# Kernel tuning notes

Measured on AMD Instinct MI355X. Metric: run time of the kernel, lower is better.

## Reference

```python
import jax, jax.numpy as jnp
import numpy as np

N0 = 292864   # input (hop-2) nodes
N1 = 11264    # hop-1 nodes
B = 1024      # target nodes
F_IN, HID, OUT = 128, 256, 47
E0, E1 = 281600, 10240
H_HIT = 146432
N_CACHE, N_GLOBAL, C_FEAT = 50000, 100000, 200000
P = 2048


def setup_inputs() -> dict:
    key = jax.random.key(0)
    ks = jax.random.split(key, 20)
    perm = jax.random.permutation(ks[0], N0)
    hit_pos = perm[:H_HIT]
    miss_pos = perm[H_HIT:]
    x = jax.random.normal(ks[1], (N0 - H_HIT, F_IN), jnp.float32)
    feat_cache = jax.random.normal(ks[2], (C_FEAT, F_IN), jnp.float32)
    hit_idx = jax.random.randint(ks[3], (H_HIT,), 0, C_FEAT)
    edge_index0 = jnp.stack([jax.random.randint(ks[4], (E0,), 0, N0),
                             jax.random.randint(ks[5], (E0,), 0, N1)])
    edge_index1 = jnp.stack([jax.random.randint(ks[6], (E1,), 0, N1),
                             jax.random.randint(ks[7], (E1,), 0, B)])
    emb_cache = jax.random.normal(ks[8], (N_CACHE, HID), jnp.float32)
    emb_cache_table = jax.random.randint(ks[9], (N_GLOBAL,), 0, N_CACHE)
    push_batch_id = jax.random.randint(ks[10], (P,), 0, N1)
    push_global_id = jax.random.randint(ks[11], (P,), 0, N_GLOBAL)
    pull_batch_id = jax.random.randint(ks[12], (P,), 0, N1)
    pull_global_id = jax.random.randint(ks[13], (P,), 0, N_GLOBAL)
    W0_l = jax.random.normal(ks[14], (F_IN, HID), jnp.float32) / np.sqrt(F_IN)
    b0_l = jnp.zeros((HID,), jnp.float32)
    W0_r = jax.random.normal(ks[15], (F_IN, HID), jnp.float32) / np.sqrt(F_IN)
    W1_l = jax.random.normal(ks[16], (HID, OUT), jnp.float32) / np.sqrt(HID)
    b1_l = jnp.zeros((OUT,), jnp.float32)
    W1_r = jax.random.normal(ks[17], (HID, OUT), jnp.float32) / np.sqrt(HID)
    return dict(x=x, feat_cache=feat_cache, emb_cache=emb_cache, hit_idx=hit_idx,
                hit_pos=hit_pos, miss_pos=miss_pos, edge_index0=edge_index0,
                edge_index1=edge_index1, emb_cache_table=emb_cache_table,
                push_batch_id=push_batch_id, push_global_id=push_global_id,
                pull_batch_id=pull_batch_id, pull_global_id=pull_global_id,
                W0_l=W0_l, b0_l=b0_l, W0_r=W0_r, W1_l=W1_l, b1_l=b1_l, W1_r=W1_r)


def _sage_conv(h_src, h_dst, edge_index, n_dst, W_l, b_l, W_r):
    # PyG SAGEConv (mean aggr): out = lin_l(mean_j x_j) + lin_r(x_i)
    src, dst = edge_index[0], edge_index[1]
    msg = h_src[src]                                              # [E, F] gather
    s = jax.ops.segment_sum(msg, dst, num_segments=n_dst)        # scatter-add
    cnt = jax.ops.segment_sum(jnp.ones((src.shape[0],), h_src.dtype), dst,
                              num_segments=n_dst)[:, None]
    mean = s / jnp.maximum(cnt, 1.0)
    return mean @ W_l + b_l + h_dst @ W_r


def reference(x, feat_cache, emb_cache, hit_idx, hit_pos, miss_pos,
              edge_index0, edge_index1, emb_cache_table,
              push_batch_id, push_global_id, pull_batch_id, pull_global_id,
              W0_l, b0_l, W0_r, W1_l, b1_l, W1_r):
    # Assemble node features from pinned feature cache (hits) + fetched feats (misses)
    h = jnp.zeros((N0, F_IN), x.dtype)
    h = h.at[hit_pos].set(feat_cache[hit_idx]).at[miss_pos].set(x)
    # Layer 0 (inner hop)
    h = _sage_conv(h, h[:N1], edge_index0, N1, W0_l, b0_l, W0_r)
    h = jax.nn.relu(h)  # dropout p=0.5 skipped (eval mode)
    # Last layer: push stale embeddings into cache, then pull cached embeddings
    slots_push = emb_cache_table[push_global_id]
    emb_cache = emb_cache.at[slots_push].set(jax.lax.stop_gradient(h[push_batch_id]))
    pulled = jax.lax.stop_gradient(emb_cache[emb_cache_table[pull_global_id]])
    h = h.at[pull_batch_id].set(pulled)
    out = _sage_conv(h, h[:B], edge_index1, B, W1_l, b1_l, W1_r)
    return jax.nn.log_softmax(out, axis=-1)
```

## Files before the change

### kernel.cpp

```cpp
#include <hip/hip_runtime.h>
#include <math.h>

#define N0c     292864
#define N1c     11264
#define Bc      1024
#define F_INc   128
#define HIDc    256
#define OUTc    47
#define E0c     281600
#define E1c     10240
#define H_HITc  146432
#define N_CACHEc 50000
#define C_FEATc 200000
#define Pc      2048

__global__ void prep_kernel(const int* __restrict__ hit_pos, const int* __restrict__ hit_idx,
                            const int* __restrict__ miss_pos, int* __restrict__ map,
                            int* __restrict__ cur0, int* __restrict__ pwin,
                            int* __restrict__ cur1, int* __restrict__ win,
                            int* __restrict__ src_row) {
  int i = blockIdx.x * 256 + threadIdx.x;
  if (i < H_HITc) {
    map[hit_pos[i]]  = hit_idx[i];
    map[miss_pos[i]] = C_FEATc + i;
  }
  if (i < N1c) { cur0[i] = 0; pwin[i] = -1; src_row[i] = i; }
  if (i < Bc)  cur1[i] = 0;
  if (i < N_CACHEc) win[i] = -1;
}

__global__ void atomics_kernel(const int* __restrict__ e0, const int* __restrict__ e1,
                               int* __restrict__ deg0, int* __restrict__ deg1,
                               const int* __restrict__ push_gid, const int* __restrict__ table,
                               int* __restrict__ win,
                               const int* __restrict__ pull_bid, int* __restrict__ pwin) {
  int i = blockIdx.x * 256 + threadIdx.x;
  if (i < E0c) {
    atomicAdd(&deg0[e0[E0c + i]], 1);
  } else if (i < E0c + E1c) {
    int j = i - E0c;
    atomicAdd(&deg1[e1[E1c + j]], 1);
  } else if (i < E0c + E1c + Pc) {
    int j = i - E0c - E1c;
    atomicMax(&win[table[push_gid[j]]], j);
  } else if (i < E0c + E1c + 2 * Pc) {
    int j = i - E0c - E1c - Pc;
    atomicMax(&pwin[pull_bid[j]], j);
  }
}

__device__ void scan_block(const int* __restrict__ deg, int* __restrict__ off,
                           int* __restrict__ cur, int n) {
  __shared__ int wsum[16];
  int tid = threadIdx.x;
  int lane = tid & 63, wid = tid >> 6;
  int ITEMS = (n + 1023) >> 10;
  int base = tid * ITEMS;
  int v[12];
  int sum = 0;
  for (int j = 0; j < ITEMS; ++j) {
    int i = base + j;
    v[j] = (i < n) ? deg[i] : 0;
    sum += v[j];
  }
  int s = sum;
  for (int o = 1; o < 64; o <<= 1) {
    int t = __shfl_up(s, o);
    if (lane >= o) s += t;
  }
  if (lane == 63) wsum[wid] = s;
  __syncthreads();
  if (tid < 16) {
    int w = wsum[tid];
    for (int o = 1; o < 16; o <<= 1) {
      int t = __shfl_up(w, o);
      if (tid >= o) w += t;
    }
    wsum[tid] = w;
  }
  __syncthreads();
  int wbase = (wid > 0) ? wsum[wid - 1] : 0;
  int run = wbase + s - sum;
  for (int j = 0; j < ITEMS; ++j) {
    int i = base + j;
    if (i < n) { off[i] = run; cur[i] = run; run += v[j]; }
  }
  if (tid == 1023) off[n] = run;
}

__global__ __launch_bounds__(1024) void scan_both_kernel(
    int* __restrict__ cur0, int* __restrict__ off0,
    int* __restrict__ cur1, int* __restrict__ off1) {
  if (blockIdx.x == 0) scan_block(cur0, off0, cur0, N1c);
  else                 scan_block(cur1, off1, cur1, Bc);
}

__global__ void scatter_resolve_kernel(const int* __restrict__ e0, const int* __restrict__ e1,
                                       const int* __restrict__ map,
                                       int* __restrict__ cur0, int* __restrict__ esrc0,
                                       int* __restrict__ cur1, int* __restrict__ esrc1,
                                       const int* __restrict__ pull_bid, const int* __restrict__ pull_gid,
                                       const int* __restrict__ table, const int* __restrict__ win,
                                       const int* __restrict__ pwin, const int* __restrict__ push_bid,
                                       int* __restrict__ src_row) {
  int i = blockIdx.x * 256 + threadIdx.x;
  if (i < E0c) {
    int p = atomicAdd(&cur0[e0[E0c + i]], 1);
    esrc0[p] = map[e0[i]];
  } else if (i < E0c + E1c) {
    int j = i - E0c;
    int p = atomicAdd(&cur1[e1[E1c + j]], 1);
    esrc1[p] = e1[j];
  } else if (i < E0c + E1c + Pc) {
    int j = i - E0c - E1c;
    int b = pull_bid[j];
    if (pwin[b] == j) {
      int slot = table[pull_gid[j]];
      int w = win[slot];
      src_row[b] = (w >= 0) ? push_bid[w] : (N1c + slot);
    }
  }
}

__global__ __launch_bounds__(256) void agg1_kernel(
    const int* __restrict__ off, const int* __restrict__ esrc,
    const float* __restrict__ fc, const float* __restrict__ x,
    float4* __restrict__ mean4) {
  __shared__ float4 sbuf[8][32];
  int d = blockIdx.x;
  int slot = threadIdx.x >> 5, lane = threadIdx.x & 31;
  int s = off[d], e = off[d + 1];
  float4 a0 = make_float4(0.f, 0.f, 0.f, 0.f);
  float4 a1 = a0, a2 = a0, a3 = a0;
  int i0 = s + slot, i1 = i0 + 8, i2 = i0 + 16, i3 = i0 + 24;
  int m0 = (i0 < e) ? esrc[i0] : -1;
  int m1 = (i1 < e) ? esrc[i1] : -1;
  int m2 = (i2 < e) ? esrc[i2] : -1;
  int m3 = (i3 < e) ? esrc[i3] : -1;
  while (i0 < e) {
    int n0 = i0 + 32, n1 = i1 + 32, n2 = i2 + 32, n3 = i3 + 32;
    int p0 = (n0 < e) ? esrc[n0] : -1;
    int p1 = (n1 < e) ? esrc[n1] : -1;
    int p2 = (n2 < e) ? esrc[n2] : -1;
    int p3 = (n3 < e) ? esrc[n3] : -1;
    {
      const float* r = (m0 < C_FEATc) ? (fc + (size_t)m0 * F_INc)
                                      : (x + (size_t)(m0 - C_FEATc) * F_INc);
      float4 v = ((const float4*)r)[lane];
      a0.x += v.x; a0.y += v.y; a0.z += v.z; a0.w += v.w;
    }
    if (i1 < e) {
      const float* r = (m1 < C_FEATc) ? (fc + (size_t)m1 * F_INc)
                                      : (x + (size_t)(m1 - C_FEATc) * F_INc);
      float4 v = ((const float4*)r)[lane];
      a1.x += v.x; a1.y += v.y; a1.z += v.z; a1.w += v.w;
    }
    if (i2 < e) {
      const float* r = (m2 < C_FEATc) ? (fc + (size_t)m2 * F_INc)
                                      : (x + (size_t)(m2 - C_FEATc) * F_INc);
      float4 v = ((const float4*)r)[lane];
      a2.x += v.x; a2.y += v.y; a2.z += v.z; a2.w += v.w;
    }
    if (i3 < e) {
      const float* r = (m3 < C_FEATc) ? (fc + (size_t)m3 * F_INc)
                                      : (x + (size_t)(m3 - C_FEATc) * F_INc);
      float4 v = ((const float4*)r)[lane];
      a3.x += v.x; a3.y += v.y; a3.z += v.z; a3.w += v.w;
    }
    i0 = n0; m0 = p0; i1 = n1; m1 = p1; i2 = n2; m2 = p2; i3 = n3; m3 = p3;
  }
  a0.x += a1.x + a2.x + a3.x;
  a0.y += a1.y + a2.y + a3.y;
  a0.z += a1.z + a2.z + a3.z;
  a0.w += a1.w + a2.w + a3.w;
  sbuf[slot][lane] = a0;
  __syncthreads();
  if (slot < 4) {
    float4 o = sbuf[slot + 4][lane];
    a0.x += o.x; a0.y += o.y; a0.z += o.z; a0.w += o.w;
    sbuf[slot][lane] = a0;
  }
  __syncthreads();
  if (slot < 2) {
    float4 o = sbuf[slot + 2][lane];
    a0.x += o.x; a0.y += o.y; a0.z += o.z; a0.w += o.w;
    sbuf[slot][lane] = a0;
  }
  __syncthreads();
  if (slot == 0) {
    float4 o = sbuf[1][lane];
    a0.x += o.x; a0.y += o.y; a0.z += o.z; a0.w += o.w;
    float inv = 1.f / fmaxf((float)(e - s), 1.f);
    mean4[(size_t)d * 32 + lane] = make_float4(a0.x * inv, a0.y * inv,
                                               a0.z * inv, a0.w * inv);
  }
}

#define ROWS1 16
__global__ __launch_bounds__(256) void gemm1_kernel(
    const float4* __restrict__ mean4, const int* __restrict__ map,
    const float* __restrict__ fc, const float* __restrict__ x,
    const float* __restrict__ W0l, const float* __restrict__ b0,
    const float* __restrict__ W0r, float* __restrict__ h1) {
  __shared__ float lin[ROWS1][256];
  int g0 = blockIdx.x * ROWS1;
  int tid = threadIdx.x;
  for (int idx = tid; idx < ROWS1 * 32; idx += 256) {
    int r = idx >> 5, l = idx & 31;
    ((float4*)&lin[r][0])[l] = mean4[(size_t)(g0 + r) * 32 + l];
  }
  for (int idx = tid; idx < ROWS1 * 32; idx += 256) {
    int r = idx >> 5, l = idx & 31;
    int m = map[g0 + r];
    const float* row = (m < C_FEATc) ? (fc + (size_t)m * F_INc)
                                     : (x + (size_t)(m - C_FEATc) * F_INc);
    ((float4*)&lin[r][128])[l] = ((const float4*)row)[l];
  }
  __syncthreads();
  int col = tid;
  float acc[ROWS1];
#pragma unroll
  for (int r = 0; r < ROWS1; ++r) acc[r] = 0.f;
  for (int kb = 0; kb < 32; ++kb) {
    float w0 = W0l[(kb * 4 + 0) * 256 + col];
    float w1 = W0l[(kb * 4 + 1) * 256 + col];
    float w2 = W0l[(kb * 4 + 2) * 256 + col];
    float w3 = W0l[(kb * 4 + 3) * 256 + col];
#pragma unroll
    for (int r = 0; r < ROWS1; ++r) {
      float4 a = *(const float4*)&lin[r][kb * 4];
      acc[r] += a.x * w0 + a.y * w1 + a.z * w2 + a.w * w3;
    }
  }
  for (int kb = 0; kb < 32; ++kb) {
    float w0 = W0r[(kb * 4 + 0) * 256 + col];
    float w1 = W0r[(kb * 4 + 1) * 256 + col];
    float w2 = W0r[(kb * 4 + 2) * 256 + col];
    float w3 = W0r[(kb * 4 + 3) * 256 + col];
#pragma unroll
    for (int r = 0; r < ROWS1; ++r) {
      float4 a = *(const float4*)&lin[r][128 + kb * 4];
      acc[r] += a.x * w0 + a.y * w1 + a.z * w2 + a.w * w3;
    }
  }
  float b = b0[col];
#pragma unroll
  for (int r = 0; r < ROWS1; ++r) {
    float v = acc[r] + b;
    h1[(size_t)(g0 + r) * HIDc + col] = v > 0.f ? v : 0.f;
  }
}

__global__ __launch_bounds__(256) void conv2_kernel(
    const int* __restrict__ off, const int* __restrict__ esrc,
    const int* __restrict__ src_row,
    const float* __restrict__ h1, const float* __restrict__ emb,
    const float* __restrict__ W1l, const float* __restrict__ b1,
    const float* __restrict__ W1r, float* __restrict__ out) {
  __shared__ float lin[512];
  __shared__ float partial[64][4];
  int row = blockIdx.x;
  int t = threadIdx.x;
  int s = off[row], e = off[row + 1];
  float acc = 0.f;
  for (int i = s; i < e; ++i) {
    int m = src_row[esrc[i]];
    const float* rp = (m < N1c) ? (h1 + (size_t)m * HIDc)
                                : (emb + (size_t)(m - N1c) * HIDc);
    acc += rp[t];
  }
  lin[t] = acc / fmaxf((float)(e - s), 1.f);
  {
    int m = src_row[row];
    const float* rp = (m < N1c) ? (h1 + (size_t)m * HIDc)
                                : (emb + (size_t)(m - N1c) * HIDc);
    lin[256 + t] = rp[t];
  }
  __syncthreads();
  int col = t >> 2;
  int seg = t & 3;
  float p = 0.f;
  if (col < OUTc) {
    int k0 = seg * 64;
    for (int k = k0; k < k0 + 64; ++k) p += lin[k] * W1l[k * OUTc + col];
    for (int k = k0; k < k0 + 64; ++k) p += lin[256 + k] * W1r[k * OUTc + col];
  }
  partial[col][seg] = p;
  __syncthreads();
  if (t < 64) {
    float v = partial[t][0] + partial[t][1] + partial[t][2] + partial[t][3];
    if (t < OUTc) v += b1[t];
    float vv = (t < OUTc) ? v : -INFINITY;
    float m = vv;
    for (int o = 32; o > 0; o >>= 1) m = fmaxf(m, __shfl_xor(m, o));
    float ex = (t < OUTc) ? expf(vv - m) : 0.f;
    float sum = ex;
    for (int o = 32; o > 0; o >>= 1) sum += __shfl_xor(sum, o);
    if (t < OUTc) out[(size_t)row * OUTc + t] = vv - m - logf(sum);
  }
}

extern "C" void kernel_launch(void* const* d_in, const int* in_sizes, int n_in,
                              void* d_out, int out_size, void* d_ws, size_t ws_size,
                              hipStream_t stream) {
  const float* x          = (const float*)d_in[0];
  const float* feat_cache = (const float*)d_in[1];
  const float* emb_cache  = (const float*)d_in[2];
  const int* hit_idx      = (const int*)d_in[3];
  const int* hit_pos      = (const int*)d_in[4];
  const int* miss_pos     = (const int*)d_in[5];
  const int* e0           = (const int*)d_in[6];
  const int* e1           = (const int*)d_in[7];
  const int* table        = (const int*)d_in[8];
  const int* push_bid     = (const int*)d_in[9];
  const int* push_gid     = (const int*)d_in[10];
  const int* pull_bid     = (const int*)d_in[11];
  const int* pull_gid     = (const int*)d_in[12];
  const float* W0l        = (const float*)d_in[13];
  const float* b0         = (const float*)d_in[14];
  const float* W0r        = (const float*)d_in[15];
  const float* W1l        = (const float*)d_in[16];
  const float* b1         = (const float*)d_in[17];
  const float* W1r        = (const float*)d_in[18];
  float* out = (float*)d_out;

  char* p = (char*)d_ws;
  size_t ob = 0;
  auto take = [&](size_t bytes) -> void* {
    void* r = p + ob;
    ob += (bytes + 255) & ~(size_t)255;
    return r;
  };
  int* MAP     = (int*)take((size_t)N0c * 4);
  int* OFF0    = (int*)take((size_t)(N1c + 1) * 4);
  int* CUR0    = (int*)take((size_t)N1c * 4);
  int* ESRC0   = (int*)take((size_t)E0c * 4);
  float* MEAN1 = (float*)take((size_t)N1c * F_INc * 4);
  float* H1    = (float*)take((size_t)N1c * HIDc * 4);
  int* WIN     = (int*)take((size_t)N_CACHEc * 4);
  int* PWIN    = (int*)take((size_t)N1c * 4);
  int* SRCROW  = (int*)take((size_t)N1c * 4);
  int* OFF1    = (int*)take((size_t)(Bc + 1) * 4);
  int* CUR1    = (int*)take((size_t)Bc * 4);
  int* ESRC1   = (int*)take((size_t)E1c * 4);

  prep_kernel<<<(H_HITc + 255) / 256, 256, 0, stream>>>(hit_pos, hit_idx, miss_pos,
                                                        MAP, CUR0, PWIN, CUR1, WIN, SRCROW);
  atomics_kernel<<<(E0c + E1c + 2 * Pc + 255) / 256, 256, 0, stream>>>(
      e0, e1, CUR0, CUR1, push_gid, table, WIN, pull_bid, PWIN);
  scan_both_kernel<<<2, 1024, 0, stream>>>(CUR0, OFF0, CUR1, OFF1);
  scatter_resolve_kernel<<<(E0c + E1c + Pc + 255) / 256, 256, 0, stream>>>(
      e0, e1, MAP, CUR0, ESRC0, CUR1, ESRC1,
      pull_bid, pull_gid, table, WIN, PWIN, push_bid, SRCROW);
  agg1_kernel<<<N1c, 256, 0, stream>>>(OFF0, ESRC0, feat_cache, x, (float4*)MEAN1);
  gemm1_kernel<<<N1c / ROWS1, 256, 0, stream>>>((const float4*)MEAN1, MAP, feat_cache, x,
                                                W0l, b0, W0r, H1);
  conv2_kernel<<<Bc, 256, 0, stream>>>(OFF1, ESRC1, SRCROW, H1, emb_cache, W1l, b1, W1r, out);
}
```

Before: 350.4 us.

## Use bf16 MFMA for layer-0 GEMM with pre-transposed packed weights

Replaces the scalar FP32 layer-0 GEMM with a matrix-core kernel built on mfma_f32_16x16x32_bf16. The prep kernel packs the concatenated W0_l/W0_r weights into a transposed bf16 buffer, and activations are converted to bf16 into shared memory. The goal is to cut the FP32 FMA cost of the 11264x256x256 GEMM, at the price of reduced input precision (bf16) and uncached global weight loads per block.

```diff
diff --git a/kernel.cpp b/kernel.cpp
--- a/kernel.cpp
+++ b/kernel.cpp
@@ -1,4 +1,5 @@
 #include <hip/hip_runtime.h>
+#include <hip/hip_bf16.h>
 #include <math.h>
 
 #define N0c     292864
@@ -14,11 +15,21 @@
 #define C_FEATc 200000
 #define Pc      2048
 
+typedef __attribute__((ext_vector_type(8))) short short8v;
+typedef __attribute__((ext_vector_type(4))) float f32x4;
+
+__device__ __forceinline__ short f2bf(float f) {
+  __hip_bfloat16 h = __float2bfloat16(f);
+  return *reinterpret_cast<short*>(&h);
+}
+
 __global__ void prep_kernel(const int* __restrict__ hit_pos, const int* __restrict__ hit_idx,
                             const int* __restrict__ miss_pos, int* __restrict__ map,
                             int* __restrict__ cur0, int* __restrict__ pwin,
                             int* __restrict__ cur1, int* __restrict__ win,
-                            int* __restrict__ src_row) {
+                            int* __restrict__ src_row,
+                            const float* __restrict__ W0l, const float* __restrict__ W0r,
+                            short* __restrict__ wt) {
   int i = blockIdx.x * 256 + threadIdx.x;
   if (i < H_HITc) {
     map[hit_pos[i]]  = hit_idx[i];
@@ -27,6 +38,13 @@
   if (i < N1c) { cur0[i] = 0; pwin[i] = -1; src_row[i] = i; }
   if (i < Bc)  cur1[i] = 0;
   if (i < N_CACHEc) win[i] = -1;
+  if (i < 32768) {
+    int col = i & 255, k = (i >> 8) * 2;
+    float v0 = (k < 128) ? W0l[k * 256 + col] : W0r[(k - 128) * 256 + col];
+    float v1 = (k + 1 < 128) ? W0l[(k + 1) * 256 + col] : W0r[(k - 127) * 256 + col];
+    short2 pk; pk.x = f2bf(v0); pk.y = f2bf(v1);
+    *reinterpret_cast<short2*>(&wt[(size_t)col * 256 + k]) = pk;
+  }
 }
 
 __global__ void atomics_kernel(const int* __restrict__ e0, const int* __restrict__ e1,
@@ -196,58 +214,60 @@
   }
 }
 
-#define ROWS1 16
-__global__ __launch_bounds__(256) void gemm1_kernel(
+__global__ __launch_bounds__(256) void gemm1_mfma_kernel(
     const float4* __restrict__ mean4, const int* __restrict__ map,
     const float* __restrict__ fc, const float* __restrict__ x,
-    const float* __restrict__ W0l, const float* __restrict__ b0,
-    const float* __restrict__ W0r, float* __restrict__ h1) {
-  __shared__ float lin[ROWS1][256];
-  int g0 = blockIdx.x * ROWS1;
+    const short* __restrict__ wt, const float* __restrict__ b0,
+    float* __restrict__ h1) {
+  __shared__ short Abf[16][264];
+  int g0 = blockIdx.x * 16;
   int tid = threadIdx.x;
-  for (int idx = tid; idx < ROWS1 * 32; idx += 256) {
+  for (int idx = tid; idx < 512; idx += 256) {
     int r = idx >> 5, l = idx & 31;
-    ((float4*)&lin[r][0])[l] = mean4[(size_t)(g0 + r) * 32 + l];
-  }
-  for (int idx = tid; idx < ROWS1 * 32; idx += 256) {
+    float4 v = mean4[(size_t)(g0 + r) * 32 + l];
+    short4 pk; pk.x = f2bf(v.x); pk.y = f2bf(v.y); pk.z = f2bf(v.z); pk.w = f2bf(v.w);
+    *reinterpret_cast<short4*>(&Abf[r][l * 4]) = pk;
+  }
+  for (int idx = tid; idx < 512; idx += 256) {
     int r = idx >> 5, l = idx & 31;
     int m = map[g0 + r];
     const float* row = (m < C_FEATc) ? (fc + (size_t)m * F_INc)
                                      : (x + (size_t)(m - C_FEATc) * F_INc);
-    ((float4*)&lin[r][128])[l] = ((const float4*)row)[l];
-  }
-  __syncthreads();
-  int col = tid;
-  float acc[ROWS1];
+    float4 v = ((const float4*)row)[l];
+    short4 pk; pk.x = f2bf(v.x); pk.y = f2bf(v.y); pk.z = f2bf(v.z); pk.w = f2bf(v.w);
+    *reinterpret_cast<short4*>(&Abf[r][128 + l * 4]) = pk;
+  }
+  __syncthreads();
+  int wave = tid >> 6, lane = tid & 63;
+  int col0 = wave * 64;
+  int lr = lane & 15;
+  int kg = lane >> 4;
+  f32x4 acc0 = {0.f, 0.f, 0.f, 0.f};
+  f32x4 acc1 = acc0, acc2 = acc0, acc3 = acc0;
 #pragma unroll
-  for (int r = 0; r < ROWS1; ++r) acc[r] = 0.f;
-  for (int kb = 0; kb < 32; ++kb) {
-    float w0 = W0l[(kb * 4 + 0) * 256 + col];
-    float w1 = W0l[(kb * 4 + 1) * 256 + col];
-    float w2 = W0l[(kb * 4 + 2) * 256 + col];
-    float w3 = W0l[(kb * 4 + 3) * 256 + col];
+  for (int ks = 0; ks < 8; ++ks) {
+    int k0 = ks * 32 + kg * 8;
+    short8v a = *reinterpret_cast<const short8v*>(&Abf[lr][k0]);
+    short8v bv0 = *reinterpret_cast<const short8v*>(&wt[(size_t)(col0 + 0  + lr) * 256 + k0]);
+    short8v bv1 = *reinterpret_cast<const short8v*>(&wt[(size_t)(col0 + 16 + lr) * 256 + k0]);
+    short8v bv2 = *reinterpret_cast<const short8v*>(&wt[(size_t)(col0 + 32 + lr) * 256 + k0]);
+    short8v bv3 = *reinterpret_cast<const short8v*>(&wt[(size_t)(col0 + 48 + lr) * 256 + k0]);
+    acc0 = __builtin_amdgcn_mfma_f32_16x16x32_bf16(a, bv0, acc0, 0, 0, 0);
+    acc1 = __builtin_amdgcn_mfma_f32_16x16x32_bf16(a, bv1, acc1, 0, 0, 0);
+    acc2 = __builtin_amdgcn_mfma_f32_16x16x32_bf16(a, bv2, acc2, 0, 0, 0);
+    acc3 = __builtin_amdgcn_mfma_f32_16x16x32_bf16(a, bv3, acc3, 0, 0, 0);
+  }
+  int rbase = kg * 4;
 #pragma unroll
-    for (int r = 0; r < ROWS1; ++r) {
-      float4 a = *(const float4*)&lin[r][kb * 4];
-      acc[r] += a.x * w0 + a.y * w1 + a.z * w2 + a.w * w3;
-    }
-  }
-  for (int kb = 0; kb < 32; ++kb) {
-    float w0 = W0r[(kb * 4 + 0) * 256 + col];
-    float w1 = W0r[(kb * 4 + 1) * 256 + col];
-    float w2 = W0r[(kb * 4 + 2) * 256 + col];
-    float w3 = W0r[(kb * 4 + 3) * 256 + col];
+  for (int nb = 0; nb < 4; ++nb) {
+    f32x4 acc = (nb == 0) ? acc0 : (nb == 1) ? acc1 : (nb == 2) ? acc2 : acc3;
+    int col = col0 + nb * 16 + lr;
+    float bias = b0[col];
 #pragma unroll
-    for (int r = 0; r < ROWS1; ++r) {
-      float4 a = *(const float4*)&lin[r][128 + kb * 4];
-      acc[r] += a.x * w0 + a.y * w1 + a.z * w2 + a.w * w3;
-    }
-  }
-  float b = b0[col];
-#pragma unroll
-  for (int r = 0; r < ROWS1; ++r) {
-    float v = acc[r] + b;
-    h1[(size_t)(g0 + r) * HIDc + col] = v > 0.f ? v : 0.f;
+    for (int r = 0; r < 4; ++r) {
+      float v = acc[r] + bias;
+      h1[(size_t)(g0 + rbase + r) * HIDc + col] = v > 0.f ? v : 0.f;
+    }
   }
 }
 
@@ -343,9 +363,11 @@
   int* OFF1    = (int*)take((size_t)(Bc + 1) * 4);
   int* CUR1    = (int*)take((size_t)Bc * 4);
   int* ESRC1   = (int*)take((size_t)E1c * 4);
+  short* WT    = (short*)take((size_t)HIDc * HIDc * 2);
 
   prep_kernel<<<(H_HITc + 255) / 256, 256, 0, stream>>>(hit_pos, hit_idx, miss_pos,
-                                                        MAP, CUR0, PWIN, CUR1, WIN, SRCROW);
+                                                        MAP, CUR0, PWIN, CUR1, WIN, SRCROW,
+                                                        W0l, W0r, WT);
   atomics_kernel<<<(E0c + E1c + 2 * Pc + 255) / 256, 256, 0, stream>>>(
       e0, e1, CUR0, CUR1, push_gid, table, WIN, pull_bid, PWIN);
   scan_both_kernel<<<2, 1024, 0, stream>>>(CUR0, OFF0, CUR1, OFF1);
@@ -353,7 +375,7 @@
       e0, e1, MAP, CUR0, ESRC0, CUR1, ESRC1,
       pull_bid, pull_gid, table, WIN, PWIN, push_bid, SRCROW);
   agg1_kernel<<<N1c, 256, 0, stream>>>(OFF0, ESRC0, feat_cache, x, (float4*)MEAN1);
-  gemm1_kernel<<<N1c / ROWS1, 256, 0, stream>>>((const float4*)MEAN1, MAP, feat_cache, x,
-                                                W0l, b0, W0r, H1);
+  gemm1_mfma_kernel<<<N1c / 16, 256, 0, stream>>>((const float4*)MEAN1, MAP, feat_cache, x,
+                                                  WT, b0, H1);
   conv2_kernel<<<Bc, 256, 0, stream>>>(OFF1, ESRC1, SRCROW, H1, emb_cache, W1l, b1, W1r, out);
 }
```

After: 323.6 us. 7.7% less time.
